# Kernel optimization log

Hardware: AMD Instinct MI355X
Metric: run time of the kernel (lower is better)

The kernel has to match this reference:

```python
import jax, jax.numpy as jnp
import numpy as np

EMBED_DIM = 1024
NUM_HEADS = 16
HEAD_DIM = EMBED_DIM // NUM_HEADS
SEQ_LEN = 4096


def setup_inputs() -> dict:
    key = jax.random.key(0)
    kx, kq, kk, kv = jax.random.split(key, 4)
    x = jax.random.normal(kx, (SEQ_LEN, EMBED_DIM), dtype=jnp.float32)
    Wq = jax.random.normal(kq, (EMBED_DIM, EMBED_DIM), dtype=jnp.float32)
    Wk = jax.random.normal(kk, (EMBED_DIM, EMBED_DIM), dtype=jnp.float32)
    Wv = jax.random.normal(kv, (EMBED_DIM, EMBED_DIM), dtype=jnp.float32)
    return {"x": x, "Wq": Wq, "Wk": Wk, "Wv": Wv}


def reference(x, Wq, Wk, Wv):
    seq_len, embed_dim = x.shape
    h, d = NUM_HEADS, HEAD_DIM
    # project then split heads: [S, E] -> [H, S, D]
    q = (x @ Wq).reshape(seq_len, h, d).transpose(1, 0, 2)
    k = (x @ Wk).reshape(seq_len, h, d).transpose(1, 0, 2)
    v = (x @ Wv).reshape(seq_len, h, d).transpose(1, 0, 2)
    # full [H, S, S] scores, scaled by sqrt(head_dim) (faithful to original)
    scores = jnp.einsum("hsd,htd->hst", q, k) / jnp.sqrt(jnp.asarray(d, dtype=q.dtype))
    weights = jax.nn.softmax(scores, axis=-1)
    out = jnp.einsum("hst,htd->hsd", weights, v)  # [H, S, D]
    return out.transpose(1, 0, 2).reshape(seq_len, embed_dim)
```

## Files before the change

### kernel.cpp

```cpp
#include <hip/hip_runtime.h>
#include <hip/hip_bf16.h>

#define SEQ 4096
#define EMB 1024
#define NHD 16
#define HDD 64

using bf16 = __hip_bfloat16;
using bf16x8 = __attribute__((ext_vector_type(8))) short;
using f32x4  = __attribute__((ext_vector_type(4))) float;
using f32x16 = __attribute__((ext_vector_type(16))) float;
using u32x4  = __attribute__((ext_vector_type(4))) unsigned int;
using u32x2  = __attribute__((ext_vector_type(2))) unsigned int;

#define MFMA16(a, b, c) __builtin_amdgcn_mfma_f32_16x16x32_bf16((a), (b), (c), 0, 0, 0)
#define MFMA32(a, b, c) __builtin_amdgcn_mfma_f32_32x32x16_bf16((a), (b), (c), 0, 0, 0)

#define QSCALE 0.1803368801111204f

__device__ __forceinline__ float b2f(bf16 b) { return __bfloat162float(b); }

__device__ __forceinline__ void gll16(const void* g, void* l) {
    __builtin_amdgcn_global_load_lds(
        (const __attribute__((address_space(1))) unsigned int*)g,
        (__attribute__((address_space(3))) unsigned int*)l, 16, 0, 0);
}

__device__ __forceinline__ unsigned pack_bf16x2(float a, float b) {
    __hip_bfloat162 p = __float22bfloat162_rn(make_float2(a, b));
    unsigned w;
    __builtin_memcpy(&w, &p, 4);
    return w;
}

__global__ void split_kernel(const float* __restrict__ src, bf16* __restrict__ hi,
                             bf16* __restrict__ lo, int n4) {
    int i = blockIdx.x * blockDim.x + threadIdx.x;
    if (i >= n4) return;
    float4 v = ((const float4*)src)[i];
    float vv[4] = {v.x, v.y, v.z, v.w};
#pragma unroll
    for (int j = 0; j < 4; j++) {
        bf16 h = __float2bfloat16(vv[j]);
        hi[i * 4 + j] = h;
        lo[i * 4 + j] = __float2bfloat16(vv[j] - b2f(h));
    }
}

__global__ void wtrans_kernel(const float* __restrict__ Wq, const float* __restrict__ Wk,
                              const float* __restrict__ Wv,
                              bf16* __restrict__ thq, bf16* __restrict__ tlq,
                              bf16* __restrict__ thk, bf16* __restrict__ tlk,
                              bf16* __restrict__ thv, bf16* __restrict__ tlv) {
    __shared__ float tile[32][33];
    const float* W;
    bf16 *wth, *wtl;
    if (blockIdx.z == 0) { W = Wq; wth = thq; wtl = tlq; }
    else if (blockIdx.z == 1) { W = Wk; wth = thk; wtl = tlk; }
    else { W = Wv; wth = thv; wtl = tlv; }
    int n0 = blockIdx.x * 32, k0 = blockIdx.y * 32;
    int tx = threadIdx.x, ty = threadIdx.y;
    for (int r = ty; r < 32; r += 8)
        tile[r][tx] = W[(k0 + r) * EMB + n0 + tx];
    __syncthreads();
    for (int r = ty; r < 32; r += 8) {
        float v = tile[tx][r];
        bf16 h = __float2bfloat16(v);
        wth[(n0 + r) * EMB + k0 + tx] = h;
        wtl[(n0 + r) * EMB + k0 + tx] = __float2bfloat16(v - b2f(h));
    }
}

template <int NTERMS>
__device__ __forceinline__ void proj_loop(
    const bf16* __restrict__ Ah, const bf16* __restrict__ Al,
    const bf16* __restrict__ Bth, const bf16* __restrict__ Btl,
    bf16* lAh, bf16* lAl, bf16* lBh, bf16* lBl,
    int m0, int n0, int t, f32x4 (&acc)[4][4]) {
    const int wid = t >> 6, lane = t & 63, lr = lane & 15, lg = lane >> 4;
    const int wr = (wid >> 1) * 64, wc = (wid & 1) * 64;
    for (int k0 = 0; k0 < EMB; k0 += 32) {
#pragma unroll
        for (int c = t; c < 512; c += 256) {
            int row = c >> 2, slot = c & 3;
            *(uint4*)&lAh[row * 40 + slot * 8] =
                *(const uint4*)&Ah[(m0 + row) * EMB + k0 + slot * 8];
            *(uint4*)&lBh[row * 40 + slot * 8] =
                *(const uint4*)&Bth[(n0 + row) * EMB + k0 + slot * 8];
            if constexpr (NTERMS == 3) {
                *(uint4*)&lAl[row * 40 + slot * 8] =
                    *(const uint4*)&Al[(m0 + row) * EMB + k0 + slot * 8];
                *(uint4*)&lBl[row * 40 + slot * 8] =
                    *(const uint4*)&Btl[(n0 + row) * EMB + k0 + slot * 8];
            }
        }
        __syncthreads();
        bf16x8 fah[4], fbh[4], fal[4], fbl[4];
#pragma unroll
        for (int i = 0; i < 4; i++) {
            fah[i] = *(const bf16x8*)&lAh[(wr + i * 16 + lr) * 40 + lg * 8];
            fbh[i] = *(const bf16x8*)&lBh[(wc + i * 16 + lr) * 40 + lg * 8];
            if constexpr (NTERMS == 3) {
                fal[i] = *(const bf16x8*)&lAl[(wr + i * 16 + lr) * 40 + lg * 8];
                fbl[i] = *(const bf16x8*)&lBl[(wc + i * 16 + lr) * 40 + lg * 8];
            }
        }
#pragma unroll
        for (int i = 0; i < 4; i++)
#pragma unroll
            for (int j = 0; j < 4; j++) {
                acc[i][j] = MFMA16(fah[i], fbh[j], acc[i][j]);
                if constexpr (NTERMS == 3) {
                    acc[i][j] = MFMA16(fah[i], fbl[j], acc[i][j]);
                    acc[i][j] = MFMA16(fal[i], fbh[j], acc[i][j]);
                }
            }
        __syncthreads();
    }
}

__global__ __launch_bounds__(256) void proj_qkv(
    const bf16* __restrict__ xh, const bf16* __restrict__ xl,
    const bf16* __restrict__ thq, const bf16* __restrict__ tlq,
    const bf16* __restrict__ thk, const bf16* __restrict__ tlk,
    const bf16* __restrict__ thv,
    bf16* __restrict__ qh, bf16* __restrict__ ql,
    bf16* __restrict__ kh, bf16* __restrict__ kl, bf16* __restrict__ vt) {
    __shared__ __align__(16) bf16 lAh[128 * 40];
    __shared__ __align__(16) bf16 lAl[128 * 40];
    __shared__ __align__(16) bf16 lBh[128 * 40];
    __shared__ __align__(16) bf16 lBl[128 * 40];
    const int t = threadIdx.x;
    const int m0 = blockIdx.y * 128;
    const int which = blockIdx.x >> 3;
    const int n0 = (blockIdx.x & 7) * 128;

    f32x4 acc[4][4];
#pragma unroll
    for (int i = 0; i < 4; i++)
#pragma unroll
        for (int j = 0; j < 4; j++) acc[i][j] = (f32x4){0.f, 0.f, 0.f, 0.f};

    if (which == 0)
        proj_loop<3>(xh, xl, thq, tlq, lAh, lAl, lBh, lBl, m0, n0, t, acc);
    else if (which == 1)
        proj_loop<3>(xh, xl, thk, tlk, lAh, lAl, lBh, lBl, m0, n0, t, acc);
    else
        proj_loop<1>(xh, xl, thv, nullptr, lAh, lAl, lBh, lBl, m0, n0, t, acc);

    const int wid = t >> 6, lane = t & 63, lr = lane & 15, lg = lane >> 4;
    const int wr = (wid >> 1) * 64, wc = (wid & 1) * 64;

    if (which == 2) {
#pragma unroll
        for (int i = 0; i < 4; i++)
#pragma unroll
            for (int j = 0; j < 4; j++) {
                int n = n0 + wc + j * 16 + lr;
                int m = m0 + wr + i * 16 + lg * 4;
                uint2 w;
                w.x = pack_bf16x2(acc[i][j][0], acc[i][j][1]);
                w.y = pack_bf16x2(acc[i][j][2], acc[i][j][3]);
                *(uint2*)&vt[(size_t)n * SEQ + m] = w;
            }
    } else {
        float scale = (which == 0) ? QSCALE : 1.0f;
        bf16* Chi = (which == 0) ? qh : kh;
        bf16* Clo = (which == 0) ? ql : kl;
#pragma unroll
        for (int i = 0; i < 4; i++)
#pragma unroll
            for (int j = 0; j < 4; j++)
#pragma unroll
                for (int q = 0; q < 4; q++) {
                    float cv = acc[i][j][q] * scale;
                    int m = m0 + wr + i * 16 + lg * 4 + q;
                    int n = n0 + wc + j * 16 + lr;
                    bf16 hv = __float2bfloat16(cv);
                    Chi[m * EMB + n] = hv;
                    Clo[m * EMB + n] = __float2bfloat16(cv - b2f(hv));
                }
    }
}

__global__ __launch_bounds__(512, 2) void attn_kernel(
    const bf16* __restrict__ qh, const bf16* __restrict__ ql,
    const bf16* __restrict__ kh, const bf16* __restrict__ kl,
    const bf16* __restrict__ vt, float* __restrict__ out) {
    __shared__ __align__(16) bf16 lKV[2][3][64 * 64];
    const int t = threadIdx.x;
    const int swz = (blockIdx.x & 7) * 32 + (blockIdx.x >> 3);
    const int h = swz >> 4;
    const int q0 = (swz & 15) * 256;
    const int wid = t >> 6, lane = t & 63;
    const int qq = lane & 31, hi = lane >> 5;
    const int qrow = q0 + wid * 32 + qq;

    bf16x8 fqh[4], fql[4];
    {
        const bf16* qbh = qh + (size_t)qrow * EMB + h * HDD + hi * 8;
        const bf16* qbl = ql + (size_t)qrow * EMB + h * HDD + hi * 8;
#pragma unroll
        for (int ds = 0; ds < 4; ds++) {
            fqh[ds] = *(const bf16x8*)(qbh + ds * 16);
            fql[ds] = *(const bf16x8*)(qbl + ds * 16);
        }
    }

    const int srow = lane >> 3, slot = lane & 7;
    const int r = wid * 8 + srow;
    const int sb = (slot ^ (r & 7)) * 16;
    const char* gp[3];
    gp[0] = (const char*)kh + ((size_t)r * EMB + h * HDD) * 2 + sb;
    gp[1] = (const char*)kl + ((size_t)r * EMB + h * HDD) * 2 + sb;
    gp[2] = (const char*)vt + ((size_t)(h * HDD + r) * SEQ) * 2 + sb;
    bf16* lp[3];
#pragma unroll
    for (int i = 0; i < 3; i++) lp[i] = &lKV[0][i][wid * 512];

    f32x16 Ofr[2];
#pragma unroll
    for (int db = 0; db < 2; db++)
#pragma unroll
        for (int rg = 0; rg < 16; rg++) Ofr[db][rg] = 0.f;
    float Mr = -1e30f, Lr = 0.f;

#pragma unroll
    for (int i = 0; i < 3; i++) {
        gll16(gp[i], lp[i]);
        gp[i] += (i < 2) ? (size_t)(64 * EMB * 2) : (size_t)(64 * 2);
    }
    __syncthreads();

    for (int tk = 0; tk < SEQ / 64; tk++) {
        const int cur = tk & 1;
        if (tk < SEQ / 64 - 1) {
#pragma unroll
            for (int i = 0; i < 3; i++) {
                gll16(gp[i], lp[i] + (cur ^ 1) * 12288);
                gp[i] += (i < 2) ? (size_t)(64 * EMB * 2) : (size_t)(64 * 2);
            }
        }
        const char* cKh = (const char*)&lKV[cur][0][0];
        const char* cKl = (const char*)&lKV[cur][1][0];
        const char* cV  = (const char*)&lKV[cur][2][0];

        __builtin_amdgcn_s_setprio(1);
        f32x16 sfr[2];
#pragma unroll
        for (int kb = 0; kb < 2; kb++) {
            const int row = kb * 32 + qq;
            const char* rbh = cKh + row * 128;
            const char* rbl = cKl + row * 128;
            const int sw = (row & 7) << 4;
            f32x16 a;
#pragma unroll
            for (int rg = 0; rg < 16; rg++) a[rg] = 0.f;
#pragma unroll
            for (int ds = 0; ds < 4; ds++) {
                const int off = (ds * 32 + hi * 16) ^ sw;
                bf16x8 kbh_ = *(const bf16x8*)(rbh + off);
                bf16x8 kbl_ = *(const bf16x8*)(rbl + off);
                a = MFMA32(kbh_, fqh[ds], a);
                a = MFMA32(kbh_, fql[ds], a);
                a = MFMA32(kbl_, fqh[ds], a);
            }
            sfr[kb] = a;
        }
        __builtin_amdgcn_s_setprio(0);

        float mx = sfr[0][0];
#pragma unroll
        for (int kb = 0; kb < 2; kb++)
#pragma unroll
            for (int rg = 0; rg < 16; rg++) mx = fmaxf(mx, sfr[kb][rg]);
        mx = fmaxf(mx, __shfl_xor(mx, 32));

        bool resc = !__all(mx <= Mr + 11.5f);
        float mn = resc ? fmaxf(Mr, mx) : Mr;
        float ps = 0.f;
#pragma unroll
        for (int kb = 0; kb < 2; kb++)
#pragma unroll
            for (int rg = 0; rg < 16; rg++) {
                float p = __builtin_exp2f(sfr[kb][rg] - mn);
                sfr[kb][rg] = p;
                ps += p;
            }
        ps += __shfl_xor(ps, 32);
        if (resc) {
            float fac = __builtin_exp2f(Mr - mn);
            Mr = mn;
            Lr = Lr * fac + ps;
#pragma unroll
            for (int db = 0; db < 2; db++)
#pragma unroll
                for (int rg = 0; rg < 16; rg++) Ofr[db][rg] *= fac;
        } else {
            Lr += ps;
        }

        bf16x8 pf[4];
#pragma unroll
        for (int sl = 0; sl < 4; sl++) {
            const int kb = sl >> 1, s8 = (sl & 1) * 8;
            unsigned w01 = pack_bf16x2(sfr[kb][s8 + 0], sfr[kb][s8 + 1]);
            unsigned w23 = pack_bf16x2(sfr[kb][s8 + 2], sfr[kb][s8 + 3]);
            unsigned w45 = pack_bf16x2(sfr[kb][s8 + 4], sfr[kb][s8 + 5]);
            unsigned w67 = pack_bf16x2(sfr[kb][s8 + 6], sfr[kb][s8 + 7]);
            u32x2 r0 = __builtin_amdgcn_permlane32_swap(w01, w45, false, false);
            u32x2 r1 = __builtin_amdgcn_permlane32_swap(w23, w67, false, false);
            u32x4 fw = {r0[0], r1[0], r0[1], r1[1]};
            bf16x8 pfv;
            __builtin_memcpy(&pfv, &fw, 16);
            pf[sl] = pfv;
        }

        __builtin_amdgcn_s_setprio(1);
#pragma unroll
        for (int sl = 0; sl < 4; sl++) {
#pragma unroll
            for (int db = 0; db < 2; db++) {
                const int vd = db * 32 + qq;
                const char* pv =
                    cV + vd * 128 + ((sl * 32 + hi * 16) ^ ((vd & 7) << 4));
                bf16x8 vf = *(const bf16x8*)pv;
                Ofr[db] = MFMA32(vf, pf[sl], Ofr[db]);
            }
        }
        __builtin_amdgcn_s_setprio(0);

        __syncthreads();
    }

    float inv = 1.0f / Lr;
    float* orow = out + (size_t)qrow * EMB + h * HDD;
#pragma unroll
    for (int db = 0; db < 2; db++)
#pragma unroll
        for (int rg = 0; rg < 4; rg++) {
            float4 o = make_float4(Ofr[db][rg * 4 + 0] * inv,
                                   Ofr[db][rg * 4 + 1] * inv,
                                   Ofr[db][rg * 4 + 2] * inv,
                                   Ofr[db][rg * 4 + 3] * inv);
            *(float4*)(orow + db * 32 + rg * 8 + hi * 4) = o;
        }
}

extern "C" void kernel_launch(void* const* d_in, const int* in_sizes, int n_in,
                              void* d_out, int out_size, void* d_ws, size_t ws_size,
                              hipStream_t stream) {
    const float* x = (const float*)d_in[0];
    const float* Wq = (const float*)d_in[1];
    const float* Wk = (const float*)d_in[2];
    const float* Wv = (const float*)d_in[3];
    float* out = (float*)d_out;

    char* ws = (char*)d_ws;
    size_t off = 0;
    auto alloc = [&](size_t elems) -> bf16* {
        bf16* p = (bf16*)(ws + off);
        off += elems * sizeof(bf16);
        return p;
    };
    bf16* xh = alloc((size_t)SEQ * EMB);
    bf16* xl = alloc((size_t)SEQ * EMB);
    bf16* wthq = alloc((size_t)EMB * EMB);
    bf16* wtlq = alloc((size_t)EMB * EMB);
    bf16* wthk = alloc((size_t)EMB * EMB);
    bf16* wtlk = alloc((size_t)EMB * EMB);
    bf16* wthv = alloc((size_t)EMB * EMB);
    bf16* wtlv = alloc((size_t)EMB * EMB);
    bf16* qh = alloc((size_t)SEQ * EMB);
    bf16* ql = alloc((size_t)SEQ * EMB);
    bf16* kh = alloc((size_t)SEQ * EMB);
    bf16* kl = alloc((size_t)SEQ * EMB);
    bf16* vt = alloc((size_t)SEQ * EMB);
    (void)ws_size; (void)in_sizes; (void)n_in; (void)out_size;

    split_kernel<<<(SEQ * EMB / 4 + 255) / 256, 256, 0, stream>>>(x, xh, xl, SEQ * EMB / 4);
    wtrans_kernel<<<dim3(32, 32, 3), dim3(32, 8), 0, stream>>>(
        Wq, Wk, Wv, wthq, wtlq, wthk, wtlk, wthv, wtlv);
    proj_qkv<<<dim3(24, 32), 256, 0, stream>>>(
        xh, xl, wthq, wtlq, wthk, wtlk, wthv, qh, ql, kh, kl, vt);
    attn_kernel<<<256, 512, 0, stream>>>(qh, ql, kh, kl, vt, out);
}
```

Before: 243.4 us.

## Merge split and weight-transpose kernels; packed-fp32 softmax and permlane reductions

Combines the x hi/lo split and the weight transpose into one prep launch and stops writing the unused Wv low-part buffer. In the attention inner loop it swaps shfl_xor for permlane32_swap in the max and sum cross-half reductions, uses tree-shaped max and sum reductions, and uses v_pk_add/v_pk_mul for the subtraction, summation and rescale steps. The aim is to cut one kernel launch and some VALU and LDS-crossbar work in the softmax. The risk is that the inline asm limits compiler scheduling and raises register pressure in the hot loop.

After: 262.5 us. +7.8%, slower.

```diff
diff --git a/kernel.cpp b/kernel.cpp
--- a/kernel.cpp
+++ b/kernel.cpp
@@ -8,6 +8,7 @@
 
 using bf16 = __hip_bfloat16;
 using bf16x8 = __attribute__((ext_vector_type(8))) short;
+using f32x2  = __attribute__((ext_vector_type(2))) float;
 using f32x4  = __attribute__((ext_vector_type(4))) float;
 using f32x16 = __attribute__((ext_vector_type(16))) float;
 using u32x4  = __attribute__((ext_vector_type(4))) unsigned int;
@@ -33,33 +34,69 @@
     return w;
 }
 
-__global__ void split_kernel(const float* __restrict__ src, bf16* __restrict__ hi,
-                             bf16* __restrict__ lo, int n4) {
-    int i = blockIdx.x * blockDim.x + threadIdx.x;
-    if (i >= n4) return;
-    float4 v = ((const float4*)src)[i];
-    float vv[4] = {v.x, v.y, v.z, v.w};
-#pragma unroll
-    for (int j = 0; j < 4; j++) {
-        bf16 h = __float2bfloat16(vv[j]);
-        hi[i * 4 + j] = h;
-        lo[i * 4 + j] = __float2bfloat16(vv[j] - b2f(h));
-    }
-}
-
-__global__ void wtrans_kernel(const float* __restrict__ Wq, const float* __restrict__ Wk,
-                              const float* __restrict__ Wv,
-                              bf16* __restrict__ thq, bf16* __restrict__ tlq,
-                              bf16* __restrict__ thk, bf16* __restrict__ tlk,
-                              bf16* __restrict__ thv, bf16* __restrict__ tlv) {
+__device__ __forceinline__ f32x2 pk_add(f32x2 a, f32x2 b) {
+    f32x2 d;
+    asm("v_pk_add_f32 %0, %1, %2" : "=v"(d) : "v"(a), "v"(b));
+    return d;
+}
+__device__ __forceinline__ f32x2 pk_mul(f32x2 a, f32x2 b) {
+    f32x2 d;
+    asm("v_pk_mul_f32 %0, %1, %2" : "=v"(d) : "v"(a), "v"(b));
+    return d;
+}
+
+__device__ __forceinline__ float xhalf_max(float x) {
+    unsigned u;
+    __builtin_memcpy(&u, &x, 4);
+    u32x2 r = __builtin_amdgcn_permlane32_swap(u, u, false, false);
+    unsigned u0 = r[0], u1 = r[1];
+    float a, b;
+    __builtin_memcpy(&a, &u0, 4);
+    __builtin_memcpy(&b, &u1, 4);
+    return fmaxf(a, b);
+}
+__device__ __forceinline__ float xhalf_sum(float x) {
+    unsigned u;
+    __builtin_memcpy(&u, &x, 4);
+    u32x2 r = __builtin_amdgcn_permlane32_swap(u, u, false, false);
+    unsigned u0 = r[0], u1 = r[1];
+    float a, b;
+    __builtin_memcpy(&a, &u0, 4);
+    __builtin_memcpy(&b, &u1, 4);
+    return a + b;
+}
+
+__global__ void prep_kernel(const float* __restrict__ x,
+                            const float* __restrict__ Wq, const float* __restrict__ Wk,
+                            const float* __restrict__ Wv,
+                            bf16* __restrict__ xh, bf16* __restrict__ xl,
+                            bf16* __restrict__ thq, bf16* __restrict__ tlq,
+                            bf16* __restrict__ thk, bf16* __restrict__ tlk,
+                            bf16* __restrict__ thv) {
     __shared__ float tile[32][33];
+    int tx = threadIdx.x, ty = threadIdx.y;
+    if (blockIdx.z == 3) {
+        int tid = (blockIdx.y * 32 + blockIdx.x) * 256 + ty * 32 + tx;
+#pragma unroll
+        for (int c = 0; c < 4; c++) {
+            int i = tid * 4 + c;
+            float4 v = ((const float4*)x)[i];
+            float vv[4] = {v.x, v.y, v.z, v.w};
+#pragma unroll
+            for (int j = 0; j < 4; j++) {
+                bf16 h = __float2bfloat16(vv[j]);
+                xh[i * 4 + j] = h;
+                xl[i * 4 + j] = __float2bfloat16(vv[j] - b2f(h));
+            }
+        }
+        return;
+    }
     const float* W;
     bf16 *wth, *wtl;
     if (blockIdx.z == 0) { W = Wq; wth = thq; wtl = tlq; }
     else if (blockIdx.z == 1) { W = Wk; wth = thk; wtl = tlk; }
-    else { W = Wv; wth = thv; wtl = tlv; }
+    else { W = Wv; wth = thv; wtl = nullptr; }
     int n0 = blockIdx.x * 32, k0 = blockIdx.y * 32;
-    int tx = threadIdx.x, ty = threadIdx.y;
     for (int r = ty; r < 32; r += 8)
         tile[r][tx] = W[(k0 + r) * EMB + n0 + tx];
     __syncthreads();
@@ -67,7 +104,8 @@
         float v = tile[tx][r];
         bf16 h = __float2bfloat16(v);
         wth[(n0 + r) * EMB + k0 + tx] = h;
-        wtl[(n0 + r) * EMB + k0 + tx] = __float2bfloat16(v - b2f(h));
+        if (wtl != nullptr)
+            wtl[(n0 + r) * EMB + k0 + tx] = __float2bfloat16(v - b2f(h));
     }
 }
 
@@ -210,6 +248,7 @@
     const int srow = lane >> 3, slot = lane & 7;
     const int r = wid * 8 + srow;
     const int sb = (slot ^ (r & 7)) * 16;
+    const size_t KSTEP = (size_t)64 * EMB * 2, VSTEP = 64 * 2;
     const char* gp[3];
     gp[0] = (const char*)kh + ((size_t)r * EMB + h * HDD) * 2 + sb;
     gp[1] = (const char*)kl + ((size_t)r * EMB + h * HDD) * 2 + sb;
@@ -228,7 +267,7 @@
 #pragma unroll
     for (int i = 0; i < 3; i++) {
         gll16(gp[i], lp[i]);
-        gp[i] += (i < 2) ? (size_t)(64 * EMB * 2) : (size_t)(64 * 2);
+        gp[i] += (i < 2) ? KSTEP : VSTEP;
     }
     __syncthreads();
 
@@ -238,7 +277,7 @@
 #pragma unroll
             for (int i = 0; i < 3; i++) {
                 gll16(gp[i], lp[i] + (cur ^ 1) * 12288);
-                gp[i] += (i < 2) ? (size_t)(64 * EMB * 2) : (size_t)(64 * 2);
+                gp[i] += (i < 2) ? KSTEP : VSTEP;
             }
         }
         const char* cKh = (const char*)&lKV[cur][0][0];
@@ -269,33 +308,57 @@
         }
         __builtin_amdgcn_s_setprio(0);
 
-        float mx = sfr[0][0];
-#pragma unroll
-        for (int kb = 0; kb < 2; kb++)
-#pragma unroll
-            for (int rg = 0; rg < 16; rg++) mx = fmaxf(mx, sfr[kb][rg]);
-        mx = fmaxf(mx, __shfl_xor(mx, 32));
+        float mA = fmaxf(fmaxf(sfr[0][0], sfr[0][1]), fmaxf(sfr[0][2], sfr[0][3]));
+        float mB = fmaxf(fmaxf(sfr[0][4], sfr[0][5]), fmaxf(sfr[0][6], sfr[0][7]));
+        float mC = fmaxf(fmaxf(sfr[0][8], sfr[0][9]), fmaxf(sfr[0][10], sfr[0][11]));
+        float mD = fmaxf(fmaxf(sfr[0][12], sfr[0][13]), fmaxf(sfr[0][14], sfr[0][15]));
+        float mE = fmaxf(fmaxf(sfr[1][0], sfr[1][1]), fmaxf(sfr[1][2], sfr[1][3]));
+        float mF = fmaxf(fmaxf(sfr[1][4], sfr[1][5]), fmaxf(sfr[1][6], sfr[1][7]));
+        float mG = fmaxf(fmaxf(sfr[1][8], sfr[1][9]), fmaxf(sfr[1][10], sfr[1][11]));
+        float mH = fmaxf(fmaxf(sfr[1][12], sfr[1][13]), fmaxf(sfr[1][14], sfr[1][15]));
+        float mx = fmaxf(fmaxf(fmaxf(mA, mB), fmaxf(mC, mD)),
+                         fmaxf(fmaxf(mE, mF), fmaxf(mG, mH)));
+        mx = xhalf_max(mx);
 
         bool resc = !__all(mx <= Mr + 11.5f);
         float mn = resc ? fmaxf(Mr, mx) : Mr;
-        float ps = 0.f;
+
+        f32x2 p[16];
+        f32x2 nm = (f32x2){-mn, -mn};
 #pragma unroll
         for (int kb = 0; kb < 2; kb++)
 #pragma unroll
-            for (int rg = 0; rg < 16; rg++) {
-                float p = __builtin_exp2f(sfr[kb][rg] - mn);
-                sfr[kb][rg] = p;
-                ps += p;
-            }
-        ps += __shfl_xor(ps, 32);
+            for (int i = 0; i < 8; i++)
+                p[kb * 8 + i] = pk_add(
+                    (f32x2){sfr[kb][2 * i], sfr[kb][2 * i + 1]}, nm);
+#pragma unroll
+        for (int i = 0; i < 16; i++) {
+            p[i][0] = __builtin_exp2f(p[i][0]);
+            p[i][1] = __builtin_exp2f(p[i][1]);
+        }
+
+        f32x2 s0 = pk_add(pk_add(p[0], p[1]), pk_add(p[2], p[3]));
+        f32x2 s1 = pk_add(pk_add(p[4], p[5]), pk_add(p[6], p[7]));
+        f32x2 s2 = pk_add(pk_add(p[8], p[9]), pk_add(p[10], p[11]));
+        f32x2 s3 = pk_add(pk_add(p[12], p[13]), pk_add(p[14], p[15]));
+        f32x2 sv = pk_add(pk_add(s0, s1), pk_add(s2, s3));
+        float ps = sv[0] + sv[1];
+        ps = xhalf_sum(ps);
+
         if (resc) {
             float fac = __builtin_exp2f(Mr - mn);
             Mr = mn;
             Lr = Lr * fac + ps;
+            f32x2 f2 = (f32x2){fac, fac};
 #pragma unroll
             for (int db = 0; db < 2; db++)
 #pragma unroll
-                for (int rg = 0; rg < 16; rg++) Ofr[db][rg] *= fac;
+                for (int i = 0; i < 8; i++) {
+                    f32x2 o = (f32x2){Ofr[db][2 * i], Ofr[db][2 * i + 1]};
+                    o = pk_mul(o, f2);
+                    Ofr[db][2 * i] = o[0];
+                    Ofr[db][2 * i + 1] = o[1];
+                }
         } else {
             Lr += ps;
         }
@@ -303,11 +366,11 @@
         bf16x8 pf[4];
 #pragma unroll
         for (int sl = 0; sl < 4; sl++) {
-            const int kb = sl >> 1, s8 = (sl & 1) * 8;
-            unsigned w01 = pack_bf16x2(sfr[kb][s8 + 0], sfr[kb][s8 + 1]);
-            unsigned w23 = pack_bf16x2(sfr[kb][s8 + 2], sfr[kb][s8 + 3]);
-            unsigned w45 = pack_bf16x2(sfr[kb][s8 + 4], sfr[kb][s8 + 5]);
-            unsigned w67 = pack_bf16x2(sfr[kb][s8 + 6], sfr[kb][s8 + 7]);
+            const int pb = sl * 4;
+            unsigned w01 = pack_bf16x2(p[pb + 0][0], p[pb + 0][1]);
+            unsigned w23 = pack_bf16x2(p[pb + 1][0], p[pb + 1][1]);
+            unsigned w45 = pack_bf16x2(p[pb + 2][0], p[pb + 2][1]);
+            unsigned w67 = pack_bf16x2(p[pb + 3][0], p[pb + 3][1]);
             u32x2 r0 = __builtin_amdgcn_permlane32_swap(w01, w45, false, false);
             u32x2 r1 = __builtin_amdgcn_permlane32_swap(w23, w67, false, false);
             u32x4 fw = {r0[0], r1[0], r0[1], r1[1]};
@@ -370,7 +433,6 @@
     bf16* wthk = alloc((size_t)EMB * EMB);
     bf16* wtlk = alloc((size_t)EMB * EMB);
     bf16* wthv = alloc((size_t)EMB * EMB);
-    bf16* wtlv = alloc((size_t)EMB * EMB);
     bf16* qh = alloc((size_t)SEQ * EMB);
     bf16* ql = alloc((size_t)SEQ * EMB);
     bf16* kh = alloc((size_t)SEQ * EMB);
@@ -378,9 +440,8 @@
     bf16* vt = alloc((size_t)SEQ * EMB);
     (void)ws_size; (void)in_sizes; (void)n_in; (void)out_size;
 
-    split_kernel<<<(SEQ * EMB / 4 + 255) / 256, 256, 0, stream>>>(x, xh, xl, SEQ * EMB / 4);
-    wtrans_kernel<<<dim3(32, 32, 3), dim3(32, 8), 0, stream>>>(
-        Wq, Wk, Wv, wthq, wtlq, wthk, wtlk, wthv, wtlv);
+    prep_kernel<<<dim3(32, 32, 4), dim3(32, 8), 0, stream>>>(
+        x, Wq, Wk, Wv, xh, xl, wthq, wtlq, wthk, wtlk, wthv);
     proj_qkv<<<dim3(24, 32), 256, 0, stream>>>(
         xh, xl, wthq, wtlq, wthk, wtlk, wthv, qh, ql, kh, kl, vt);
     attn_kernel<<<256, 512, 0, stream>>>(qh, ql, kh, kl, vt, out);
```
